# Optimization experiments

Measured on AMD Instinct MI355X. Metric: run time of the kernel, lower is better.

## Reference

```python
import jax, jax.numpy as jnp
import numpy as np

HEADS = 12

def setup_inputs() -> dict:
    key = jax.random.key(0)
    k1, k2, k3 = jax.random.split(key, 3)
    b, n, d = 8, 1024, 768
    x = jax.random.normal(k1, (b, n, d), dtype=jnp.float32)
    # xavier_uniform-like init for linear weights
    lim_qkv = float(np.sqrt(6.0 / (d + 3 * d)))
    W_qkv = jax.random.uniform(k2, (3 * d, d), dtype=jnp.float32, minval=-lim_qkv, maxval=lim_qkv)
    b_qkv = jnp.zeros((3 * d,), dtype=jnp.float32)
    lim_o = float(np.sqrt(6.0 / (d + d)))
    W_out = jax.random.uniform(k3, (d, d), dtype=jnp.float32, minval=-lim_o, maxval=lim_o)
    b_out = jnp.zeros((d,), dtype=jnp.float32)
    return {"x": x, "W_qkv": W_qkv, "b_qkv": b_qkv, "W_out": W_out, "b_out": b_out}

def reference(x, W_qkv, b_qkv, W_out, b_out):
    b, n, d = x.shape
    h = HEADS
    hd = d // h
    scale = d ** (-0.5)  # NOTE: original scales by dim**-0.5, not head_dim**-0.5
    qkv = x @ W_qkv.T + b_qkv                      # [b, n, 3d]
    q, k, v = jnp.split(qkv, 3, axis=-1)           # each [b, n, d]
    def to_heads(t):
        return t.reshape(b, n, h, hd).transpose(0, 2, 1, 3)  # [b, h, n, hd]
    q, k, v = to_heads(q), to_heads(k), to_heads(v)
    dots = jnp.einsum('bhid,bhjd->bhij', q, k) * scale       # [b, h, n, n]
    attn = jax.nn.softmax(dots, axis=-1)
    out = jnp.einsum('bhij,bhjd->bhid', attn, v)             # [b, h, n, hd]
    out = out.transpose(0, 2, 1, 3).reshape(b, n, d)
    return out @ W_out.T + b_out
```

## Files before the change

kernel.cpp:

```cpp
#include <hip/hip_runtime.h>
#include <stdint.h>

typedef __bf16 bf16x8 __attribute__((ext_vector_type(8)));
typedef float  f32x4  __attribute__((ext_vector_type(4)));
typedef unsigned short u16;

#define AS1 __attribute__((address_space(1)))
#define AS3 __attribute__((address_space(3)))
#define G2L(gp, lp) __builtin_amdgcn_global_load_lds( \
    (const AS1 unsigned int*)(uintptr_t)(gp), \
    (AS3 unsigned int*)(uintptr_t)(lp), 16, 0, 0)

static __device__ __forceinline__ u16 f32_to_bf16(float f) {
    unsigned u = __float_as_uint(f);
    u += 0x7fffu + ((u >> 16) & 1u);
    return (u16)(u >> 16);
}

static __device__ __forceinline__ unsigned pack_bf16(float lo, float hi) {
    return (unsigned)f32_to_bf16(lo) | ((unsigned)f32_to_bf16(hi) << 16);
}

static __device__ __forceinline__ float fast_exp2(float x) {
    return __builtin_amdgcn_exp2f(x);
}

static __device__ __forceinline__ f32x4 mfma16(bf16x8 a, bf16x8 b, f32x4 c) {
    return __builtin_amdgcn_mfma_f32_16x16x32_bf16(a, b, c, 0, 0, 0);
}

__global__ void cvt3_k(const float* __restrict__ a, const float* __restrict__ b,
                       const float* __restrict__ c, u16* __restrict__ out) {
    const int i = blockIdx.x * blockDim.x + threadIdx.x;
    const float* src; int off;
    if (i < 1572864)      { src = a; off = 0; }
    else if (i < 2015232) { src = b; off = 1572864; }
    else                  { src = c; off = 2015232; }
    const float4 v = reinterpret_cast<const float4*>(src)[i - off];
    reinterpret_cast<uint2*>(out)[i] = make_uint2(pack_bf16(v.x, v.y), pack_bf16(v.z, v.w));
}

template<int OUTF32>
__global__ __launch_bounds__(256, 2) void gemm_bt_k(const u16* __restrict__ A, const u16* __restrict__ B,
                                                    const float* __restrict__ bias, void* __restrict__ Cp,
                                                    int M, int N, int K, int nbx, int qcols, float qsc) {
    __shared__ __align__(16) u16 As[2][128 * 64];
    __shared__ __align__(16) u16 Bs[2][128 * 64];
    const int id = blockIdx.x;
    const int cpx = gridDim.x >> 3;
    const int swz = (id & 7) * cpx + (id >> 3);
    const int bx = swz % nbx, by = swz / nbx;
    const int t = threadIdx.x, w = t >> 6, l = t & 63, lr = l & 15, lg = l >> 4;
    const int wr = w >> 1, wc = w & 1;
    const long rowBase = (long)by * 128;
    const long colBase = (long)bx * 128;

    const f32x4 z = {0.f, 0.f, 0.f, 0.f};
    f32x4 acc[4][4];
    #pragma unroll
    for (int m = 0; m < 4; ++m)
        #pragma unroll
        for (int n = 0; n < 4; ++n) acc[m][n] = z;

    const int kSteps = K >> 6;
    #pragma unroll
    for (int i = 0; i < 4; ++i) {
        const int c = i * 256 + t, row = c >> 3, ch = c & 7;
        const int sch = ch ^ (row & 7);
        G2L(A + (rowBase + row) * K + sch * 8, &As[0][(i * 256 + w * 64) * 8]);
        G2L(B + (colBase + row) * K + sch * 8, &Bs[0][(i * 256 + w * 64) * 8]);
    }
    for (int kt = 0; kt < kSteps; ++kt) {
        const int cur = kt & 1;
        asm volatile("s_waitcnt vmcnt(0)" ::: "memory");
        __builtin_amdgcn_sched_barrier(0);
        __builtin_amdgcn_s_barrier();
        __builtin_amdgcn_sched_barrier(0);
        if (kt + 1 < kSteps) {
            const int k0 = (kt + 1) << 6;
            #pragma unroll
            for (int i = 0; i < 4; ++i) {
                const int c = i * 256 + t, row = c >> 3, ch = c & 7;
                const int sch = ch ^ (row & 7);
                G2L(A + (rowBase + row) * K + k0 + sch * 8, &As[cur ^ 1][(i * 256 + w * 64) * 8]);
                G2L(B + (colBase + row) * K + k0 + sch * 8, &Bs[cur ^ 1][(i * 256 + w * 64) * 8]);
            }
        }
        __builtin_amdgcn_sched_barrier(0);
        #pragma unroll
        for (int kk = 0; kk < 2; ++kk) {
            bf16x8 af[4], bfr[4];
            #pragma unroll
            for (int m = 0; m < 4; ++m) {
                const int row = wr * 64 + m * 16 + lr;
                af[m] = *reinterpret_cast<const bf16x8*>(&As[cur][row * 64 + (((kk * 4 + lg) ^ (lr & 7)) << 3)]);
            }
            #pragma unroll
            for (int n = 0; n < 4; ++n) {
                const int row = wc * 64 + n * 16 + lr;
                bfr[n] = *reinterpret_cast<const bf16x8*>(&Bs[cur][row * 64 + (((kk * 4 + lg) ^ (lr & 7)) << 3)]);
            }
            #pragma unroll
            for (int m = 0; m < 4; ++m)
                #pragma unroll
                for (int n = 0; n < 4; ++n) acc[m][n] = mfma16(af[m], bfr[n], acc[m][n]);
        }
    }
    #pragma unroll
    for (int n = 0; n < 4; ++n) {
        const long gc = colBase + wc * 64 + n * 16 + lr;
        const float bv = bias[gc];
        const float csc = (gc < qcols) ? qsc : 1.0f;
        #pragma unroll
        for (int m = 0; m < 4; ++m) {
            const long gr = rowBase + wr * 64 + m * 16 + lg * 4;
            #pragma unroll
            for (int r = 0; r < 4; ++r) {
                const float v = (acc[m][n][r] + bv) * csc;
                if (OUTF32) reinterpret_cast<float*>(Cp)[(gr + r) * N + gc] = v;
                else        reinterpret_cast<u16*>(Cp)[(gr + r) * N + gc] = f32_to_bf16(v);
            }
        }
    }
}

__global__ __launch_bounds__(256) void transpose_v_k(const u16* __restrict__ qkv, u16* __restrict__ vt) {
    const int bh = blockIdx.y, b = bh / 12, h = bh % 12;
    const int nt = blockIdx.x;
    __shared__ __align__(16) u16 Ts[64][72];
    const int t = threadIdx.x;
    const int rr = t >> 2;
    #pragma unroll
    for (int i = 0; i < 2; ++i) {
        const int ch = (t & 3) + i * 4;
        const u16* src = qkv + (long)(b * 1024 + nt * 64 + rr) * 2304 + 1536 + h * 64 + ch * 8;
        *reinterpret_cast<uint4*>(&Ts[rr][ch * 8]) = *reinterpret_cast<const uint4*>(src);
    }
    __syncthreads();
    #pragma unroll
    for (int i = 0; i < 2; ++i) {
        const int ch = (t & 3) + i * 4;
        u16 vals[8];
        #pragma unroll
        for (int j = 0; j < 8; ++j)
            vals[j] = Ts[(ch >> 2) * 32 + (j >> 2) * 16 + (ch & 3) * 4 + (j & 3)][rr];
        u16* dst = vt + (long)(bh * 64 + rr) * 1024 + nt * 64 + ch * 8;
        *reinterpret_cast<uint4*>(dst) = *reinterpret_cast<const uint4*>(vals);
    }
}

__global__ __launch_bounds__(256, 3) void attn_k(const u16* __restrict__ qkv, const u16* __restrict__ vt,
                                                 u16* __restrict__ outp) {
    const int id = blockIdx.x;
    const int bh = id % 96, qt = id / 96;
    const int b = bh / 12, h = bh % 12;
    const int t = threadIdx.x, w = t >> 6, l = t & 63, lr = l & 15, lg = l >> 4;
    __shared__ __align__(16) u16 Ks[2][64 * 64];
    __shared__ __align__(16) u16 Vts[2][64 * 64];

    const u16* kb = qkv + 768 + h * 64;
    const u16* vb = vt + (long)bh * 64 * 1024;

    #pragma unroll
    for (int i = 0; i < 2; ++i) {
        const int c = (i * 4 + w) * 64 + l;
        const int row = c >> 3, sch = (c & 7) ^ (row & 7);
        G2L(kb + (long)(b * 1024 + row) * 2304 + sch * 8, &Ks[0][(i * 4 + w) * 512]);
        G2L(vb + (long)row * 1024 + sch * 8, &Vts[0][(i * 4 + w) * 512]);
    }
    const u16* qb = qkv + (long)(b * 1024 + qt * 128 + w * 32) * 2304 + h * 64;
    bf16x8 aq[2][2];
    #pragma unroll
    for (int qf = 0; qf < 2; ++qf)
        #pragma unroll
        for (int kk = 0; kk < 2; ++kk)
            aq[qf][kk] = *reinterpret_cast<const bf16x8*>(qb + (long)(qf * 16 + lr) * 2304 + (kk * 4 + lg) * 8);

    const f32x4 z = {0.f, 0.f, 0.f, 0.f};
    f32x4 o[2][4];
    f32x4 dacc[2];
    #pragma unroll
    for (int qf = 0; qf < 2; ++qf) {
        #pragma unroll
        for (int n = 0; n < 4; ++n) o[qf][n] = z;
        dacc[qf] = z;
    }
    const unsigned one2 = 0x3F803F80u;
    uint4 onesu = make_uint4(one2, one2, one2, one2);
    const bf16x8 ones = *reinterpret_cast<const bf16x8*>(&onesu);

    #pragma unroll 2
    for (int kt = 0; kt < 16; ++kt) {
        const int cur = kt & 1;
        asm volatile("s_waitcnt vmcnt(0)" ::: "memory");
        __builtin_amdgcn_sched_barrier(0);
        __builtin_amdgcn_s_barrier();
        __builtin_amdgcn_sched_barrier(0);
        if (kt < 15) {
            const int ktn = kt + 1;
            #pragma unroll
            for (int i = 0; i < 2; ++i) {
                const int c = (i * 4 + w) * 64 + l;
                const int row = c >> 3, sch = (c & 7) ^ (row & 7);
                G2L(kb + (long)(b * 1024 + ktn * 64 + row) * 2304 + sch * 8, &Ks[cur ^ 1][(i * 4 + w) * 512]);
                G2L(vb + (long)row * 1024 + ktn * 64 + sch * 8, &Vts[cur ^ 1][(i * 4 + w) * 512]);
            }
        }
        __builtin_amdgcn_sched_barrier(0);
        f32x4 s[4][2];
        #pragma unroll
        for (int kc = 0; kc < 4; ++kc)
            #pragma unroll
            for (int qf = 0; qf < 2; ++qf) s[kc][qf] = z;
        #pragma unroll
        for (int kk = 0; kk < 2; ++kk) {
            #pragma unroll
            for (int kc = 0; kc < 4; ++kc) {
                const int row = kc * 16 + lr;
                bf16x8 bk = *reinterpret_cast<const bf16x8*>(&Ks[cur][row * 64 + (((kk * 4 + lg) ^ (lr & 7)) << 3)]);
                s[kc][0] = mfma16(bk, aq[0][kk], s[kc][0]);
                s[kc][1] = mfma16(bk, aq[1][kk], s[kc][1]);
            }
        }
        #pragma unroll
        for (int qf = 0; qf < 2; ++qf) {
            float pv[4][4];
            #pragma unroll
            for (int kc = 0; kc < 4; ++kc)
                #pragma unroll
                for (int r = 0; r < 4; ++r)
                    pv[kc][r] = fast_exp2(s[kc][qf][r]);
            uint4 u0, u1;
            u0.x = pack_bf16(pv[0][0], pv[0][1]); u0.y = pack_bf16(pv[0][2], pv[0][3]);
            u0.z = pack_bf16(pv[1][0], pv[1][1]); u0.w = pack_bf16(pv[1][2], pv[1][3]);
            u1.x = pack_bf16(pv[2][0], pv[2][1]); u1.y = pack_bf16(pv[2][2], pv[2][3]);
            u1.z = pack_bf16(pv[3][0], pv[3][1]); u1.w = pack_bf16(pv[3][2], pv[3][3]);
            bf16x8 pa0 = *reinterpret_cast<bf16x8*>(&u0);
            bf16x8 pa1 = *reinterpret_cast<bf16x8*>(&u1);
            dacc[qf] = mfma16(pa0, ones, dacc[qf]);
            dacc[qf] = mfma16(pa1, ones, dacc[qf]);
            #pragma unroll
            for (int kk = 0; kk < 2; ++kk) {
                const bf16x8 pa = kk ? pa1 : pa0;
                const int swzk = ((kk * 4 + lg) ^ (lr & 7)) << 3;
                #pragma unroll
                for (int n = 0; n < 4; ++n) {
                    const int row = n * 16 + lr;
                    bf16x8 vbf = *reinterpret_cast<const bf16x8*>(&Vts[cur][row * 64 + swzk]);
                    o[qf][n] = mfma16(pa, vbf, o[qf][n]);
                }
            }
        }
    }
    #pragma unroll
    for (int qf = 0; qf < 2; ++qf) {
        const int qrow = qt * 128 + w * 32 + qf * 16 + lg * 4;
        #pragma unroll
        for (int r = 0; r < 4; ++r) {
            const float inv = 1.0f / dacc[qf][r];
            #pragma unroll
            for (int n = 0; n < 4; ++n) {
                outp[(long)(b * 1024 + qrow + r) * 768 + h * 64 + n * 16 + lr] =
                    f32_to_bf16(o[qf][n][r] * inv);
            }
        }
    }
}

extern "C" void kernel_launch(void* const* d_in, const int* in_sizes, int n_in,
                              void* d_out, int out_size, void* d_ws, size_t ws_size,
                              hipStream_t stream) {
    (void)in_sizes; (void)n_in; (void)out_size; (void)ws_size;
    const float* x    = (const float*)d_in[0];
    const float* Wqkv = (const float*)d_in[1];
    const float* bqkv = (const float*)d_in[2];
    const float* Wout = (const float*)d_in[3];
    const float* bout = (const float*)d_in[4];

    u16* xb   = (u16*)d_ws;
    u16* Wqb  = xb  + 6291456;
    u16* Wob  = Wqb + 1769472;
    u16* qkv  = Wob + 589824;
    u16* vtb  = qkv + 18874368;
    u16* attn = vtb + 6291456;

    const float sc2 = 0.052058773f;

    cvt3_k<<<8448, 256, 0, stream>>>(x, Wqkv, Wout, xb);

    gemm_bt_k<0><<<1152, 256, 0, stream>>>(xb, Wqb, bqkv, qkv, 8192, 2304, 768, 18, 768, sc2);
    transpose_v_k<<<dim3(16, 96), 256, 0, stream>>>(qkv, vtb);
    attn_k<<<768, 256, 0, stream>>>(qkv, vtb, attn);
    gemm_bt_k<1><<<384, 256, 0, stream>>>(attn, Wob, bout, d_out, 8192, 768, 768, 6, 0, 1.0f);
}
```

Measured before the change: 102.8 us.

## Use three-stage K=32 LDS pipeline in GEMM kernel with higher occupancy

Replaces the double-buffered K=64 tile loop in the bf16 GEMM with a triple-buffered K=32 pipeline that prefetches two stages ahead and waits with a partial vmcnt instead of draining all loads. LDS per block shrinks, so launch bounds are raised to three blocks per CU to hide global-memory latency better. The LDS swizzle is adapted to 32-wide rows. In exchange there are twice as many barriers per K, less MFMA work per barrier, and more register pressure under the tighter launch bound.

```diff
diff --git a/kernel.cpp b/kernel.cpp
--- a/kernel.cpp
+++ b/kernel.cpp
@@ -41,11 +41,11 @@
 }
 
 template<int OUTF32>
-__global__ __launch_bounds__(256, 2) void gemm_bt_k(const u16* __restrict__ A, const u16* __restrict__ B,
+__global__ __launch_bounds__(256, 3) void gemm_bt_k(const u16* __restrict__ A, const u16* __restrict__ B,
                                                     const float* __restrict__ bias, void* __restrict__ Cp,
                                                     int M, int N, int K, int nbx, int qcols, float qsc) {
-    __shared__ __align__(16) u16 As[2][128 * 64];
-    __shared__ __align__(16) u16 Bs[2][128 * 64];
+    __shared__ __align__(16) u16 As[3][128 * 32];
+    __shared__ __align__(16) u16 Bs[3][128 * 32];
     const int id = blockIdx.x;
     const int cpx = gridDim.x >> 3;
     const int swz = (id & 7) * cpx + (id >> 3);
@@ -62,50 +62,48 @@
         #pragma unroll
         for (int n = 0; n < 4; ++n) acc[m][n] = z;
 
-    const int kSteps = K >> 6;
-    #pragma unroll
-    for (int i = 0; i < 4; ++i) {
-        const int c = i * 256 + t, row = c >> 3, ch = c & 7;
-        const int sch = ch ^ (row & 7);
-        G2L(A + (rowBase + row) * K + sch * 8, &As[0][(i * 256 + w * 64) * 8]);
-        G2L(B + (colBase + row) * K + sch * 8, &Bs[0][(i * 256 + w * 64) * 8]);
-    }
+    const int kSteps = K >> 5;
+
+    #define STAGE_G(kt, bi) do {                                                   \
+        const int k0_ = (kt) << 5;                                                 \
+        _Pragma("unroll")                                                          \
+        for (int i_ = 0; i_ < 2; ++i_) {                                           \
+            const int c_ = i_ * 256 + t, row_ = c_ >> 2, ch_ = c_ & 3;             \
+            const int sch_ = ch_ ^ ((row_ >> 1) & 3);                              \
+            G2L(A + (rowBase + row_) * K + k0_ + sch_ * 8, &As[bi][(i_ * 256 + w * 64) * 8]); \
+            G2L(B + (colBase + row_) * K + k0_ + sch_ * 8, &Bs[bi][(i_ * 256 + w * 64) * 8]); \
+        }                                                                          \
+    } while (0)
+
+    STAGE_G(0, 0);
+    STAGE_G(1, 1);
     for (int kt = 0; kt < kSteps; ++kt) {
-        const int cur = kt & 1;
-        asm volatile("s_waitcnt vmcnt(0)" ::: "memory");
+        const int cur = kt % 3;
+        if (kt + 1 < kSteps) asm volatile("s_waitcnt vmcnt(4)" ::: "memory");
+        else                 asm volatile("s_waitcnt vmcnt(0)" ::: "memory");
         __builtin_amdgcn_sched_barrier(0);
         __builtin_amdgcn_s_barrier();
         __builtin_amdgcn_sched_barrier(0);
-        if (kt + 1 < kSteps) {
-            const int k0 = (kt + 1) << 6;
-            #pragma unroll
-            for (int i = 0; i < 4; ++i) {
-                const int c = i * 256 + t, row = c >> 3, ch = c & 7;
-                const int sch = ch ^ (row & 7);
-                G2L(A + (rowBase + row) * K + k0 + sch * 8, &As[cur ^ 1][(i * 256 + w * 64) * 8]);
-                G2L(B + (colBase + row) * K + k0 + sch * 8, &Bs[cur ^ 1][(i * 256 + w * 64) * 8]);
-            }
-        }
-        __builtin_amdgcn_sched_barrier(0);
-        #pragma unroll
-        for (int kk = 0; kk < 2; ++kk) {
-            bf16x8 af[4], bfr[4];
-            #pragma unroll
-            for (int m = 0; m < 4; ++m) {
-                const int row = wr * 64 + m * 16 + lr;
-                af[m] = *reinterpret_cast<const bf16x8*>(&As[cur][row * 64 + (((kk * 4 + lg) ^ (lr & 7)) << 3)]);
-            }
-            #pragma unroll
-            for (int n = 0; n < 4; ++n) {
-                const int row = wc * 64 + n * 16 + lr;
-                bfr[n] = *reinterpret_cast<const bf16x8*>(&Bs[cur][row * 64 + (((kk * 4 + lg) ^ (lr & 7)) << 3)]);
-            }
-            #pragma unroll
-            for (int m = 0; m < 4; ++m)
-                #pragma unroll
-                for (int n = 0; n < 4; ++n) acc[m][n] = mfma16(af[m], bfr[n], acc[m][n]);
-        }
-    }
+        if (kt + 2 < kSteps) STAGE_G(kt + 2, (kt + 2) % 3);
+        __builtin_amdgcn_sched_barrier(0);
+        bf16x8 af[4], bfr[4];
+        #pragma unroll
+        for (int m = 0; m < 4; ++m) {
+            const int row = wr * 64 + m * 16 + lr;
+            af[m] = *reinterpret_cast<const bf16x8*>(&As[cur][row * 32 + ((lg ^ ((row >> 1) & 3)) << 3)]);
+        }
+        #pragma unroll
+        for (int n = 0; n < 4; ++n) {
+            const int row = wc * 64 + n * 16 + lr;
+            bfr[n] = *reinterpret_cast<const bf16x8*>(&Bs[cur][row * 32 + ((lg ^ ((row >> 1) & 3)) << 3)]);
+        }
+        #pragma unroll
+        for (int m = 0; m < 4; ++m)
+            #pragma unroll
+            for (int n = 0; n < 4; ++n) acc[m][n] = mfma16(af[m], bfr[n], acc[m][n]);
+    }
+    #undef STAGE_G
+
     #pragma unroll
     for (int n = 0; n < 4; ++n) {
         const long gc = colBase + wc * 64 + n * 16 + lr;
```

New measurement: 110.1 us. +7.1%, slower.

## Fuse V transpose into QKV GEMM epilogue and raise attention occupancy

Applied to the files above, without the earlier changes.

The QKV projection GEMM now writes the V columns straight into the transposed, permuted vt buffer, using packed 8-byte stores. This replaces the separate transpose_v_k kernel, which cost an extra launch plus a read and write of V. The V section of the qkv buffer is no longer written. The attention kernel's launch bounds also change from 3 to 4 blocks per SIMD, which may cause register spills.

```diff
diff --git a/kernel.cpp b/kernel.cpp
--- a/kernel.cpp
+++ b/kernel.cpp
@@ -43,6 +43,7 @@
 template<int OUTF32>
 __global__ __launch_bounds__(256, 2) void gemm_bt_k(const u16* __restrict__ A, const u16* __restrict__ B,
                                                     const float* __restrict__ bias, void* __restrict__ Cp,
+                                                    u16* __restrict__ vtp,
                                                     int M, int N, int K, int nbx, int qcols, float qsc) {
     __shared__ __align__(16) u16 As[2][128 * 64];
     __shared__ __align__(16) u16 Bs[2][128 * 64];
@@ -113,43 +114,30 @@
         const float csc = (gc < qcols) ? qsc : 1.0f;
         #pragma unroll
         for (int m = 0; m < 4; ++m) {
-            const long gr = rowBase + wr * 64 + m * 16 + lg * 4;
-            #pragma unroll
-            for (int r = 0; r < 4; ++r) {
-                const float v = (acc[m][n][r] + bv) * csc;
-                if (OUTF32) reinterpret_cast<float*>(Cp)[(gr + r) * N + gc] = v;
-                else        reinterpret_cast<u16*>(Cp)[(gr + r) * N + gc] = f32_to_bf16(v);
-            }
-        }
-    }
-}
-
-__global__ __launch_bounds__(256) void transpose_v_k(const u16* __restrict__ qkv, u16* __restrict__ vt) {
-    const int bh = blockIdx.y, b = bh / 12, h = bh % 12;
-    const int nt = blockIdx.x;
-    __shared__ __align__(16) u16 Ts[64][72];
-    const int t = threadIdx.x;
-    const int rr = t >> 2;
-    #pragma unroll
-    for (int i = 0; i < 2; ++i) {
-        const int ch = (t & 3) + i * 4;
-        const u16* src = qkv + (long)(b * 1024 + nt * 64 + rr) * 2304 + 1536 + h * 64 + ch * 8;
-        *reinterpret_cast<uint4*>(&Ts[rr][ch * 8]) = *reinterpret_cast<const uint4*>(src);
-    }
-    __syncthreads();
-    #pragma unroll
-    for (int i = 0; i < 2; ++i) {
-        const int ch = (t & 3) + i * 4;
-        u16 vals[8];
-        #pragma unroll
-        for (int j = 0; j < 8; ++j)
-            vals[j] = Ts[(ch >> 2) * 32 + (j >> 2) * 16 + (ch & 3) * 4 + (j & 3)][rr];
-        u16* dst = vt + (long)(bh * 64 + rr) * 1024 + nt * 64 + ch * 8;
-        *reinterpret_cast<uint4*>(dst) = *reinterpret_cast<const uint4*>(vals);
-    }
-}
-
-__global__ __launch_bounds__(256, 3) void attn_k(const u16* __restrict__ qkv, const u16* __restrict__ vt,
+            const long gr0 = rowBase + wr * 64 + m * 16 + lg * 4;
+            if (vtp != nullptr && gc >= 1536) {
+                const int hh = (int)(gc - 1536) >> 6;
+                const int dd = (int)(gc - 1536) & 63;
+                const long bb = gr0 >> 10;
+                const int t64 = (int)((gr0 & 1023) >> 6);
+                const int pbase = (m >> 1) * 32 + lg * 8 + (m & 1) * 4;
+                const unsigned w0 = pack_bf16(acc[m][n][0] + bv, acc[m][n][1] + bv);
+                const unsigned w1 = pack_bf16(acc[m][n][2] + bv, acc[m][n][3] + bv);
+                u16* dst = vtp + ((bb * 12 + hh) * 64 + dd) * 1024L + t64 * 64 + pbase;
+                *reinterpret_cast<uint2*>(dst) = make_uint2(w0, w1);
+            } else {
+                #pragma unroll
+                for (int r = 0; r < 4; ++r) {
+                    const float v = (acc[m][n][r] + bv) * csc;
+                    if (OUTF32) reinterpret_cast<float*>(Cp)[(gr0 + r) * N + gc] = v;
+                    else        reinterpret_cast<u16*>(Cp)[(gr0 + r) * N + gc] = f32_to_bf16(v);
+                }
+            }
+        }
+    }
+}
+
+__global__ __launch_bounds__(256, 4) void attn_k(const u16* __restrict__ qkv, const u16* __restrict__ vt,
                                                  u16* __restrict__ outp) {
     const int id = blockIdx.x;
     const int bh = id % 96, qt = id / 96;
@@ -288,8 +276,7 @@
 
     cvt3_k<<<8448, 256, 0, stream>>>(x, Wqkv, Wout, xb);
 
-    gemm_bt_k<0><<<1152, 256, 0, stream>>>(xb, Wqb, bqkv, qkv, 8192, 2304, 768, 18, 768, sc2);
-    transpose_v_k<<<dim3(16, 96), 256, 0, stream>>>(qkv, vtb);
+    gemm_bt_k<0><<<1152, 256, 0, stream>>>(xb, Wqb, bqkv, qkv, vtb, 8192, 2304, 768, 18, 768, sc2);
     attn_k<<<768, 256, 0, stream>>>(qkv, vtb, attn);
-    gemm_bt_k<1><<<384, 256, 0, stream>>>(attn, Wob, bout, d_out, 8192, 768, 768, 6, 0, 1.0f);
-}
+    gemm_bt_k<1><<<384, 256, 0, stream>>>(attn, Wob, bout, d_out, nullptr, 8192, 768, 768, 6, 0, 1.0f);
+}
```

New measurement: 111.8 us. +8.8%, slower.
